# Optimization experiments

Measured on AMD Instinct MI355X. Metric: run time of the kernel, lower is better.

The kernel has to match this reference:

```python
import jax, jax.numpy as jnp
import numpy as np

INPUT_SIZE = 512
LATENT = 256
NUM_PROTOTYPES = 128
NUM_CLASSES = 8
PC = NUM_PROTOTYPES // NUM_CLASSES  # prototypes per class
EPS = 1e-4
LOG_MIN = float(np.log(1e-8))  # clamp bounds for logVar


def setup_inputs() -> dict:
    key = jax.random.key(0)
    ks = jax.random.split(key, 12)
    B = 16384
    s = 0.05
    return {
        "x_tab": jax.random.normal(ks[0], (B, INPUT_SIZE), jnp.float32),
        "t": jax.random.randint(ks[1], (B,), 0, NUM_CLASSES),
        "prototype_vectors": jax.random.normal(ks[2], (NUM_PROTOTYPES, LATENT), jnp.float32),
        "W1": jax.random.normal(ks[3], (2 * LATENT, INPUT_SIZE), jnp.float32) * s,
        "b1": jnp.zeros((2 * LATENT,), jnp.float32),
        "W2": jax.random.normal(ks[4], (2 * LATENT, 2 * LATENT), jnp.float32) * s,
        "b2": jnp.zeros((2 * LATENT,), jnp.float32),
        "Wd1": jax.random.normal(ks[5], (LATENT, LATENT), jnp.float32) * s,
        "bd1": jnp.zeros((LATENT,), jnp.float32),
        "Wd2": jax.random.normal(ks[6], (INPUT_SIZE, LATENT), jnp.float32) * s,
        "bd2": jnp.zeros((INPUT_SIZE,), jnp.float32),
        "W_last": jax.random.normal(ks[7], (1, NUM_PROTOTYPES), jnp.float32) * s,
    }


def reference(x_tab, t, prototype_vectors, W1, b1, W2, b2, Wd1, bd1, Wd2, bd2, W_last):
    B = x_tab.shape[0]
    # encoder MLP: Linear -> ReLU -> Linear, output [B, 2*latent]
    h = jnp.maximum(x_tab @ W1.T + b1, 0.0)
    conv = h @ W2.T + b2
    mu = conv[:, :LATENT]
    logVar = jnp.clip(conv[:, LATENT:], LOG_MIN, -LOG_MIN)
    z = mu  # test=True path: z = mu (deterministic)

    # per-sample indices of the prototypes of the correct class: [B, PC]
    idx = t[:, None] * PC + jnp.arange(PC)[None, :]
    protos = prototype_vectors[idx]  # [B, PC, L] gather

    # cdist (p=2) + log-similarity
    diff = z[:, None, :] - protos  # [B, PC, L]
    d = jnp.sqrt(jnp.sum(diff * diff, axis=-1))  # [B, PC]
    sim = jnp.log((d + 1.0) / (d + EPS))

    # scatter into full [B, P] sparse sim tensor
    full_sim = jnp.zeros((B, NUM_PROTOTYPES), x_tab.dtype).at[
        jnp.arange(B)[:, None], idx].set(sim)

    # KL(N(mu, exp(logVar/2)) || N(p, 1)) per-dim, mean over latent
    var = jnp.exp(logVar)
    kl = jnp.mean(-0.5 * logVar[:, None, :]
                  + 0.5 * (var[:, None, :] + diff * diff)
                  - 0.5, axis=-1)  # [B, PC]
    klw = kl * sim
    mask = (klw > 0).astype(sim.dtype)
    kl_loss = jnp.mean(jnp.sum(klw, axis=1) / jnp.sum(sim * mask, axis=1))

    out = full_sim @ W_last.T  # [B, 1]

    # decoder: Linear -> ReLU -> Linear -> tanh
    dh = jnp.maximum(z @ Wd1.T + bd1, 0.0)
    decoded = jnp.tanh(dh @ Wd2.T + bd2)

    # ortho loss over per-class prototype blocks
    pk = prototype_vectors.reshape(NUM_CLASSES, PC, LATENT)
    pk = pk - jnp.mean(pk, axis=1, keepdims=True)
    gram = jnp.einsum('cil,cjl->cij', pk, pk) - jnp.eye(PC, dtype=pk.dtype)
    ortho_loss = jnp.mean(jnp.sqrt(jnp.sum(gram * gram, axis=(1, 2))))

    return out, decoded, kl_loss, ortho_loss
```

## Files before the change

kernel.cpp:

```cpp
#include <hip/hip_runtime.h>
#include <math.h>

typedef unsigned short u16;
typedef unsigned int   u32;
typedef _Float16 f16;
typedef f16   f16x4 __attribute__((ext_vector_type(4)));
typedef f16   f16x8 __attribute__((ext_vector_type(8)));
typedef float f32x4 __attribute__((ext_vector_type(4)));

#define B_ROWS 16384
#define PC 16
#define EPS_SIM 1e-4f
#define LOG_MIN_F (-18.420680743952367f)
#define KL_IDX  (B_ROWS + B_ROWS * 512)
#define OR_IDX  (KL_IDX + 1)

#define GLD16(gp, lp) __builtin_amdgcn_global_load_lds( \
    (const __attribute__((address_space(1))) void*)(gp), \
    (__attribute__((address_space(3))) void*)(lp), 16, 0, 0)

__device__ __forceinline__ void conv4(const float* __restrict__ src,
                                      f16* __restrict__ dst, int i)
{
    float4 v = ((const float4*)src)[i];
    f16x4 o = { (f16)v.x, (f16)v.y, (f16)v.z, (f16)v.w };
    ((f16x4*)dst)[i] = o;
}

__global__ __launch_bounds__(256)
void prep_kernel(const float* __restrict__ x,   const float* __restrict__ W1,
                 const float* __restrict__ W2,  const float* __restrict__ Wd1,
                 const float* __restrict__ Wd2, const float* __restrict__ protos,
                 f16* __restrict__ x_h,  f16* __restrict__ W1h,
                 f16* __restrict__ W2h,  f16* __restrict__ Wd1h,
                 f16* __restrict__ Wd2h, f16* __restrict__ ph,
                 float* __restrict__ pnorm, float* __restrict__ opart,
                 float* __restrict__ S, float* __restrict__ Mn,
                 float* __restrict__ out)
{
    __shared__ float pk[PC][257];
    __shared__ float red[256];
    int blk = blockIdx.x, t = threadIdx.x;

    if (blk < 8) {
        int c = blk;
        for (int i = t; i < PC * 256; i += 256)
            pk[i >> 8][i & 255] = protos[c * PC * 256 + i];
        __syncthreads();
        float mean = 0.f;
#pragma unroll
        for (int i = 0; i < PC; ++i) mean += pk[i][t];
        mean *= (1.f / (float)PC);
#pragma unroll
        for (int i = 0; i < PC; ++i) pk[i][t] -= mean;
        __syncthreads();
        int i = t >> 4, j = t & 15;
        float gg = 0.f;
#pragma unroll 8
        for (int l = 0; l < 256; ++l) gg = fmaf(pk[i][l], pk[j][l], gg);
        gg -= (i == j) ? 1.f : 0.f;
        red[t] = gg * gg;
        __syncthreads();
        for (int s = 128; s; s >>= 1) { if (t < s) red[t] += red[t + s]; __syncthreads(); }
        if (t == 0) opart[c] = sqrtf(red[0]);
        return;
    }
    int b2 = blk - 8;
    if (b2 < 8192)         conv4(x,   x_h,  b2 * 256 + t);
    else if (b2 < 8448)    conv4(W1,  W1h,  (b2 - 8192) * 256 + t);
    else if (b2 < 8704)    conv4(W2,  W2h,  (b2 - 8448) * 256 + t);
    else if (b2 < 8768)    conv4(Wd1, Wd1h, (b2 - 8704) * 256 + t);
    else if (b2 < 8896)    conv4(Wd2, Wd2h, (b2 - 8768) * 256 + t);
    else if (b2 < 8928)    conv4(protos, ph, (b2 - 8896) * 256 + t);
    else if (b2 < 8930) {
        int tt = (b2 - 8928) * 256 + t;
        int row = tt >> 2, q = tt & 3;
        const float* pr = protos + (size_t)row * 256 + q * 64;
        float s = 0.f;
#pragma unroll
        for (int j = 0; j < 16; ++j) {
            float4 v = *(const float4*)(pr + j * 4);
            float r0 = (float)(f16)v.x, r1 = (float)(f16)v.y;
            float r2 = (float)(f16)v.z, r3 = (float)(f16)v.w;
            s = fmaf(r0, r0, s); s = fmaf(r1, r1, s);
            s = fmaf(r2, r2, s); s = fmaf(r3, r3, s);
        }
        s += __shfl_xor(s, 1, 64);
        s += __shfl_xor(s, 2, 64);
        if (q == 0) pnorm[row] = s;
    } else {
        int i = (b2 - 8930) * 256 + t;
        S[i] = 0.f; Mn[i] = 0.f;
        if (i == 0) out[KL_IDX] = 0.f;
    }
}

template<int MODE, int KK>
__global__ __launch_bounds__(256, 2)
void gemm_mfma(const f16* __restrict__ A, const f16* __restrict__ B,
               const f16* __restrict__ P, const float* __restrict__ bias,
               f16* __restrict__ C16, float* __restrict__ Cf,
               float* __restrict__ Srow, float* __restrict__ Mnorm,
               f16* __restrict__ Xc, int ldc)
{
    __shared__ __align__(16) f16 LA[128][32];
    __shared__ __align__(16) f16 LB[128][32];

    const int t = threadIdx.x, lane = t & 63, wave = t >> 6;
    const int wm = wave >> 1, wn = wave & 1;
    const int bm = blockIdx.x * 128;
    const int y  = blockIdx.y;
    const bool proto = (MODE == 5) && (y == 2);
    const int bn  = y * 128;
    const int bnB = proto ? 0 : bn;
    const f16* Bp = proto ? P : B;
    const int rA = lane & 15, g = lane >> 4;
    const int srow = lane >> 2, cp = lane & 3;

    f32x4 acc[4][4];
    const f32x4 z4 = {0.f, 0.f, 0.f, 0.f};
#pragma unroll
    for (int i = 0; i < 4; ++i)
#pragma unroll
        for (int j = 0; j < 4; ++j) acc[i][j] = z4;

    auto stage = [&](int kt) {
#pragma unroll
        for (int s = 0; s < 2; ++s) {
            int row = wave * 32 + s * 16 + srow;
            int lc  = (cp - (row >> 1)) & 3;
            GLD16(A  + (size_t)(bm  + row) * KK + kt * 32 + lc * 8,
                  &LA[wave * 32 + s * 16][0]);
            GLD16(Bp + (size_t)(bnB + row) * KK + kt * 32 + lc * 8,
                  &LB[wave * 32 + s * 16][0]);
        }
    };

    constexpr int T = KK / 32;
    stage(0);
    for (int tk = 0; tk < T; ++tk) {
        __syncthreads();

        f16x8 a[4], b[4];
#pragma unroll
        for (int i = 0; i < 4; ++i) {
            int m = wm * 64 + i * 16 + rA;
            int c = ((g + (m >> 1)) & 3) * 8;
            a[i] = *(const f16x8*)&LA[m][c];
            int n = wn * 64 + i * 16 + rA;
            int cn = ((g + (n >> 1)) & 3) * 8;
            b[i] = *(const f16x8*)&LB[n][cn];
        }

        __syncthreads();
        if (tk + 1 < T) stage(tk + 1);

#pragma unroll
        for (int i = 0; i < 4; ++i)
#pragma unroll
            for (int j = 0; j < 4; ++j)
                acc[i][j] = __builtin_amdgcn_mfma_f32_16x16x32_f16(a[i], b[j], acc[i][j], 0, 0, 0);
    }

    if (proto) {
#pragma unroll
        for (int i = 0; i < 4; ++i)
#pragma unroll
            for (int r = 0; r < 4; ++r) {
                size_t row = bm + wm * 64 + i * 16 + g * 4 + r;
#pragma unroll
                for (int j = 0; j < 4; ++j) {
                    int col = wn * 64 + j * 16 + rA;
                    Xc[row * 128 + col] = (f16)acc[i][j][r];
                }
            }
        return;
    }

    float bv[4];
#pragma unroll
    for (int j = 0; j < 4; ++j) bv[j] = bias[bn + wn * 64 + j * 16 + rA];

    if (MODE == 4 && y >= 2) {
#pragma unroll
        for (int i = 0; i < 4; ++i)
#pragma unroll
            for (int r = 0; r < 4; ++r) {
                int row = bm + wm * 64 + i * 16 + g * 4 + r;
                float s = 0.f;
#pragma unroll
                for (int j = 0; j < 4; ++j) {
                    float lv = acc[i][j][r] + bv[j];
                    lv = fminf(fmaxf(lv, LOG_MIN_F), -LOG_MIN_F);
                    s += 0.5f * __expf(lv) - 0.5f * lv - 0.5f;
                }
                s += __shfl_xor(s, 1, 64); s += __shfl_xor(s, 2, 64);
                s += __shfl_xor(s, 4, 64); s += __shfl_xor(s, 8, 64);
                if (rA == 0) atomicAdd(&Srow[row], s * (1.f / 256.f));
            }
        return;
    }

#pragma unroll
    for (int i = 0; i < 4; ++i)
#pragma unroll
        for (int r = 0; r < 4; ++r) {
            size_t row = bm + wm * 64 + i * 16 + g * 4 + r;
            float sq = 0.f;
#pragma unroll
            for (int j = 0; j < 4; ++j) {
                int col = bn + wn * 64 + j * 16 + rA;
                float v = acc[i][j][r] + bv[j];
                if (MODE == 0 || MODE == 5) v = fmaxf(v, 0.f);
                if (MODE == 3) {
                    float e = __expf(2.f * v);
                    Cf[row * ldc + col] = 1.f - 2.f / (e + 1.f);
                } else {
                    f16 hv = (f16)v;
                    C16[row * ldc + col] = hv;
                    if (MODE == 4) {
                        float vr = (float)hv;
                        sq = fmaf(vr, vr, sq);
                    }
                }
            }
            if (MODE == 4) {
                sq += __shfl_xor(sq, 1, 64); sq += __shfl_xor(sq, 2, 64);
                sq += __shfl_xor(sq, 4, 64); sq += __shfl_xor(sq, 8, 64);
                if (rA == 0) atomicAdd(&Mnorm[row], sq);
            }
        }
}

__global__ __launch_bounds__(256)
void proto_finish(const f16* __restrict__ Xc, const float* __restrict__ Mnorm,
                  const float* __restrict__ Sr, const int* __restrict__ tcls,
                  const float* __restrict__ pnorm, const float* __restrict__ Wlast,
                  const float* __restrict__ opart,
                  float* __restrict__ out, float* __restrict__ kl_out)
{
    __shared__ float pnS[128], wlS[128], red[4];
    int t = threadIdx.x;
    if (t < 128) { pnS[t] = pnorm[t]; wlS[t] = Wlast[t]; }
    __syncthreads();

    int b = blockIdx.x * 256 + t;
    int cls = tcls[b];
    float Mn = Mnorm[b], Sb = Sr[b];
    const f16* xr = Xc + (size_t)b * 128 + cls * 16;
    f16x8 c0 = *(const f16x8*)xr;
    f16x8 c1 = *(const f16x8*)(xr + 8);

    float num = 0.f, den = 0.f, ov = 0.f;
#pragma unroll
    for (int p = 0; p < 16; ++p) {
        float c  = (p < 8) ? (float)c0[p] : (float)c1[p - 8];
        int  ip  = cls * 16 + p;
        float dd = fmaxf(Mn + pnS[ip] - 2.f * c, 0.f);
        float d  = sqrtf(dd);
        float sim = __logf((d + 1.f) / (d + EPS_SIM));
        float kl  = Sb + dd * (0.5f / 256.f);
        float klw = kl * sim;
        num += klw;
        den += (klw > 0.f) ? sim : 0.f;
        ov  += sim * wlS[ip];
    }
    out[b] = ov;

    float v = num / den;
#pragma unroll
    for (int off = 32; off; off >>= 1) v += __shfl_xor(v, off, 64);
    int lane = t & 63, w = t >> 6;
    if (lane == 0) red[w] = v;
    __syncthreads();
    if (t == 0)
        atomicAdd(kl_out, (red[0] + red[1] + red[2] + red[3]) * (1.f / (float)B_ROWS));
    if (blockIdx.x == 0 && t == 0) {
        float o = 0.f;
#pragma unroll
        for (int c8 = 0; c8 < 8; ++c8) o += opart[c8];
        out[OR_IDX] = o * (1.f / 8.f);
    }
}

extern "C" void kernel_launch(void* const* d_in, const int* in_sizes, int n_in,
                              void* d_out, int out_size, void* d_ws, size_t ws_size,
                              hipStream_t stream)
{
    const float* x      = (const float*)d_in[0];
    const int*   tcls   = (const int*)  d_in[1];
    const float* protos = (const float*)d_in[2];
    const float* W1     = (const float*)d_in[3];
    const float* b1     = (const float*)d_in[4];
    const float* W2     = (const float*)d_in[5];
    const float* b2     = (const float*)d_in[6];
    const float* Wd1    = (const float*)d_in[7];
    const float* bd1    = (const float*)d_in[8];
    const float* Wd2    = (const float*)d_in[9];
    const float* bd2    = (const float*)d_in[10];
    const float* Wlast  = (const float*)d_in[11];

    float* out     = (float*)d_out;
    float* decoded = out + B_ROWS;

    f16* h_h = (f16*)decoded;

    f16* wsf  = (f16*)d_ws;
    f16* x_h  = wsf;
    f16* mu_h = wsf + 8388608;
    f16* dh_h = wsf + 12582912;

    float* S = (float*)((char*)d_ws + 33554432);
    f16* w = (f16*)(S + 32768);
    f16 *W1h = w, *W2h = w + 262144, *Wd1h = w + 524288, *Wd2h = w + 589824;
    f16 *ph  = w + 720896;
    float* munorm = (float*)(w + 753664);
    float* pnorm  = munorm + 16384;
    float* opart  = pnorm + 128;
    f16* Xc = (f16*)((char*)d_ws + 37748736);

    hipLaunchKernelGGL(prep_kernel, dim3(9002), dim3(256), 0, stream,
                       x, W1, W2, Wd1, Wd2, protos,
                       x_h, W1h, W2h, Wd1h, Wd2h, ph,
                       pnorm, opart, S, munorm, out);

    hipLaunchKernelGGL((gemm_mfma<0, 512>), dim3(128, 4), dim3(256), 0, stream,
                       x_h, W1h, (f16*)nullptr, b1,
                       h_h, (float*)nullptr, (float*)nullptr, (float*)nullptr,
                       (f16*)nullptr, 512);
    hipLaunchKernelGGL((gemm_mfma<4, 512>), dim3(128, 4), dim3(256), 0, stream,
                       h_h, W2h, (f16*)nullptr, b2,
                       mu_h, (float*)nullptr, S, munorm,
                       (f16*)nullptr, 256);
    hipLaunchKernelGGL((gemm_mfma<5, 256>), dim3(128, 3), dim3(256), 0, stream,
                       mu_h, Wd1h, ph, bd1,
                       dh_h, (float*)nullptr, (float*)nullptr, (float*)nullptr,
                       Xc, 256);
    hipLaunchKernelGGL(proto_finish, dim3(64), dim3(256), 0, stream,
                       Xc, munorm, S, tcls, pnorm, Wlast, opart,
                       out, out + KL_IDX);
    hipLaunchKernelGGL((gemm_mfma<3, 256>), dim3(128, 4), dim3(256), 0, stream,
                       dh_h, Wd2h, (f16*)nullptr, bd2,
                       (f16*)nullptr, decoded, (float*)nullptr, (float*)nullptr,
                       (f16*)nullptr, 512);
}
```

Baseline: 77.05 us.

## Fuse fp32 input conversion into first GEMM, double-buffer LDS, merge proto_finish

The first GEMM now reads x in fp32 directly and converts it to fp16 into swizzled LDS. This removes the separate x conversion pass and its 16 MB workspace round trip. GEMM tiles shrink to 128x64 with double-buffered LDS, one barrier per k-step and launch bounds raised to 4 blocks per CU, giving more blocks and better overlap. The proto_finish kernel is folded into the decoder GEMM launch as an extra grid row, saving one launch. The trade-offs are A tiles reloaded twice as often, register-staged conversion loads instead of async LDS loads, and extra branching in the GEMM kernel.

```diff
diff --git a/kernel.cpp b/kernel.cpp
--- a/kernel.cpp
+++ b/kernel.cpp
@@ -1,8 +1,6 @@
 #include <hip/hip_runtime.h>
 #include <math.h>
 
-typedef unsigned short u16;
-typedef unsigned int   u32;
 typedef _Float16 f16;
 typedef f16   f16x4 __attribute__((ext_vector_type(4)));
 typedef f16   f16x8 __attribute__((ext_vector_type(8)));
@@ -28,12 +26,12 @@
 }
 
 __global__ __launch_bounds__(256)
-void prep_kernel(const float* __restrict__ x,   const float* __restrict__ W1,
-                 const float* __restrict__ W2,  const float* __restrict__ Wd1,
-                 const float* __restrict__ Wd2, const float* __restrict__ protos,
-                 f16* __restrict__ x_h,  f16* __restrict__ W1h,
-                 f16* __restrict__ W2h,  f16* __restrict__ Wd1h,
-                 f16* __restrict__ Wd2h, f16* __restrict__ ph,
+void prep_kernel(const float* __restrict__ W1,  const float* __restrict__ W2,
+                 const float* __restrict__ Wd1, const float* __restrict__ Wd2,
+                 const float* __restrict__ protos,
+                 f16* __restrict__ W1h,  f16* __restrict__ W2h,
+                 f16* __restrict__ Wd1h, f16* __restrict__ Wd2h,
+                 f16* __restrict__ ph,
                  float* __restrict__ pnorm, float* __restrict__ opart,
                  float* __restrict__ S, float* __restrict__ Mn,
                  float* __restrict__ out)
@@ -66,14 +64,13 @@
         return;
     }
     int b2 = blk - 8;
-    if (b2 < 8192)         conv4(x,   x_h,  b2 * 256 + t);
-    else if (b2 < 8448)    conv4(W1,  W1h,  (b2 - 8192) * 256 + t);
-    else if (b2 < 8704)    conv4(W2,  W2h,  (b2 - 8448) * 256 + t);
-    else if (b2 < 8768)    conv4(Wd1, Wd1h, (b2 - 8704) * 256 + t);
-    else if (b2 < 8896)    conv4(Wd2, Wd2h, (b2 - 8768) * 256 + t);
-    else if (b2 < 8928)    conv4(protos, ph, (b2 - 8896) * 256 + t);
-    else if (b2 < 8930) {
-        int tt = (b2 - 8928) * 256 + t;
+    if (b2 < 256)          conv4(W1,  W1h,  b2 * 256 + t);
+    else if (b2 < 512)     conv4(W2,  W2h,  (b2 - 256) * 256 + t);
+    else if (b2 < 576)     conv4(Wd1, Wd1h, (b2 - 512) * 256 + t);
+    else if (b2 < 704)     conv4(Wd2, Wd2h, (b2 - 576) * 256 + t);
+    else if (b2 < 736)     conv4(protos, ph, (b2 - 704) * 256 + t);
+    else if (b2 < 738) {
+        int tt = (b2 - 736) * 256 + t;
         int row = tt >> 2, q = tt & 3;
         const float* pr = protos + (size_t)row * 256 + q * 64;
         float s = 0.f;
@@ -89,77 +86,175 @@
         s += __shfl_xor(s, 2, 64);
         if (q == 0) pnorm[row] = s;
     } else {
-        int i = (b2 - 8930) * 256 + t;
+        int i = (b2 - 738) * 256 + t;
         S[i] = 0.f; Mn[i] = 0.f;
         if (i == 0) out[KL_IDX] = 0.f;
     }
 }
 
-template<int MODE, int KK>
-__global__ __launch_bounds__(256, 2)
-void gemm_mfma(const f16* __restrict__ A, const f16* __restrict__ B,
-               const f16* __restrict__ P, const float* __restrict__ bias,
+template<int MODE, int KK, int CONV>
+__global__ __launch_bounds__(256, 4)
+void gemm_mfma(const float* __restrict__ A32, const f16* __restrict__ A,
+               const f16* __restrict__ B, const f16* __restrict__ P,
+               const float* __restrict__ bias,
                f16* __restrict__ C16, float* __restrict__ Cf,
                float* __restrict__ Srow, float* __restrict__ Mnorm,
-               f16* __restrict__ Xc, int ldc)
+               f16* __restrict__ Xc,
+               const int* __restrict__ tcls, const float* __restrict__ pnorm,
+               const float* __restrict__ Wlast, const float* __restrict__ opart,
+               float* __restrict__ out, float* __restrict__ kl_out, int ldc)
 {
-    __shared__ __align__(16) f16 LA[128][32];
-    __shared__ __align__(16) f16 LB[128][32];
-
-    const int t = threadIdx.x, lane = t & 63, wave = t >> 6;
+    const int t = threadIdx.x;
+
+    if (MODE == 3 && blockIdx.y == 8) {
+        if (blockIdx.x >= 64) return;
+        __shared__ float pnS[128], wlS[128], redk[4];
+        if (t < 128) { pnS[t] = pnorm[t]; wlS[t] = Wlast[t]; }
+        __syncthreads();
+        int b = blockIdx.x * 256 + t;
+        int cls = tcls[b];
+        float Mn = Mnorm[b], Sb = Srow[b];
+        const f16* xr = Xc + (size_t)b * 128 + cls * 16;
+        f16x8 c0 = *(const f16x8*)xr;
+        f16x8 c1 = *(const f16x8*)(xr + 8);
+        float num = 0.f, den = 0.f, ov = 0.f;
+#pragma unroll
+        for (int p = 0; p < 16; ++p) {
+            float c  = (p < 8) ? (float)c0[p] : (float)c1[p - 8];
+            int  ip  = cls * 16 + p;
+            float dd = fmaxf(Mn + pnS[ip] - 2.f * c, 0.f);
+            float d  = sqrtf(dd);
+            float sim = __logf((d + 1.f) / (d + EPS_SIM));
+            float kl  = Sb + dd * (0.5f / 256.f);
+            float klw = kl * sim;
+            num += klw;
+            den += (klw > 0.f) ? sim : 0.f;
+            ov  += sim * wlS[ip];
+        }
+        out[b] = ov;
+        float v = num / den;
+#pragma unroll
+        for (int off = 32; off; off >>= 1) v += __shfl_xor(v, off, 64);
+        int lane2 = t & 63, w2 = t >> 6;
+        if (lane2 == 0) redk[w2] = v;
+        __syncthreads();
+        if (t == 0)
+            atomicAdd(kl_out, (redk[0] + redk[1] + redk[2] + redk[3]) * (1.f / (float)B_ROWS));
+        if (blockIdx.x == 0 && t == 0) {
+            float o = 0.f;
+#pragma unroll
+            for (int c8 = 0; c8 < 8; ++c8) o += opart[c8];
+            out[OR_IDX] = o * (1.f / 8.f);
+        }
+        return;
+    }
+
+    __shared__ __align__(16) f16 LA[2][128][32];
+    __shared__ __align__(16) f16 LB[2][64][32];
+
+    const int lane = t & 63, wave = t >> 6;
     const int wm = wave >> 1, wn = wave & 1;
     const int bm = blockIdx.x * 128;
     const int y  = blockIdx.y;
-    const bool proto = (MODE == 5) && (y == 2);
-    const int bn  = y * 128;
-    const int bnB = proto ? 0 : bn;
+    const bool proto = (MODE == 5) && (y >= 4);
+    const int bn  = y * 64;
+    const int bnB = proto ? (y - 4) * 64 : bn;
     const f16* Bp = proto ? P : B;
     const int rA = lane & 15, g = lane >> 4;
     const int srow = lane >> 2, cp = lane & 3;
 
-    f32x4 acc[4][4];
+    f32x4 acc[4][2];
     const f32x4 z4 = {0.f, 0.f, 0.f, 0.f};
 #pragma unroll
     for (int i = 0; i < 4; ++i)
 #pragma unroll
-        for (int j = 0; j < 4; ++j) acc[i][j] = z4;
-
-    auto stage = [&](int kt) {
-#pragma unroll
-        for (int s = 0; s < 2; ++s) {
-            int row = wave * 32 + s * 16 + srow;
-            int lc  = (cp - (row >> 1)) & 3;
-            GLD16(A  + (size_t)(bm  + row) * KK + kt * 32 + lc * 8,
-                  &LA[wave * 32 + s * 16][0]);
-            GLD16(Bp + (size_t)(bnB + row) * KK + kt * 32 + lc * 8,
-                  &LB[wave * 32 + s * 16][0]);
-        }
-    };
+        for (int j = 0; j < 2; ++j) acc[i][j] = z4;
 
     constexpr int T = KK / 32;
-    stage(0);
+
+    {
+        int row = wave * 16 + srow;
+        int lc  = (cp - (row >> 1)) & 3;
+        GLD16(Bp + (size_t)(bnB + row) * KK + lc * 8, &LB[0][wave * 16][0]);
+        if (CONV) {
+#pragma unroll
+            for (int s = 0; s < 4; ++s) {
+                int r8 = wave * 32 + s * 8 + (lane >> 3);
+                int h  = lane & 7;
+                float4 v = *(const float4*)(A32 + (size_t)(bm + r8) * KK + h * 4);
+                f16x4 o = {(f16)v.x, (f16)v.y, (f16)v.z, (f16)v.w};
+                *(f16x4*)((char*)&LA[0][r8][0] +
+                          ((((h >> 1) + (r8 >> 1)) & 3) * 16 + (h & 1) * 8)) = o;
+            }
+        } else {
+#pragma unroll
+            for (int s = 0; s < 2; ++s) {
+                int r16 = wave * 32 + s * 16 + srow;
+                int lc2 = (cp - (r16 >> 1)) & 3;
+                GLD16(A + (size_t)(bm + r16) * KK + lc2 * 8,
+                      &LA[0][wave * 32 + s * 16][0]);
+            }
+        }
+    }
+
     for (int tk = 0; tk < T; ++tk) {
-        __syncthreads();
-
-        f16x8 a[4], b[4];
+        const int buf = tk & 1;
+        __syncthreads();
+
+        f16x8 a[4], b[2];
 #pragma unroll
         for (int i = 0; i < 4; ++i) {
             int m = wm * 64 + i * 16 + rA;
             int c = ((g + (m >> 1)) & 3) * 8;
-            a[i] = *(const f16x8*)&LA[m][c];
-            int n = wn * 64 + i * 16 + rA;
-            int cn = ((g + (n >> 1)) & 3) * 8;
-            b[i] = *(const f16x8*)&LB[n][cn];
-        }
-
-        __syncthreads();
-        if (tk + 1 < T) stage(tk + 1);
+            a[i] = *(const f16x8*)&LA[buf][m][c];
+        }
+#pragma unroll
+        for (int j = 0; j < 2; ++j) {
+            int n = wn * 32 + j * 16 + rA;
+            int c = ((g + (n >> 1)) & 3) * 8;
+            b[j] = *(const f16x8*)&LB[buf][n][c];
+        }
+
+        float4 rr[4];
+        if (tk + 1 < T) {
+            int row = wave * 16 + srow;
+            int lc  = (cp - (row >> 1)) & 3;
+            GLD16(Bp + (size_t)(bnB + row) * KK + (tk + 1) * 32 + lc * 8,
+                  &LB[buf ^ 1][wave * 16][0]);
+            if (CONV) {
+#pragma unroll
+                for (int s = 0; s < 4; ++s) {
+                    int r8 = wave * 32 + s * 8 + (lane >> 3);
+                    rr[s] = *(const float4*)(A32 + (size_t)(bm + r8) * KK +
+                                             (tk + 1) * 32 + (lane & 7) * 4);
+                }
+            } else {
+#pragma unroll
+                for (int s = 0; s < 2; ++s) {
+                    int r16 = wave * 32 + s * 16 + srow;
+                    int lc2 = (cp - (r16 >> 1)) & 3;
+                    GLD16(A + (size_t)(bm + r16) * KK + (tk + 1) * 32 + lc2 * 8,
+                          &LA[buf ^ 1][wave * 32 + s * 16][0]);
+                }
+            }
+        }
 
 #pragma unroll
         for (int i = 0; i < 4; ++i)
 #pragma unroll
-            for (int j = 0; j < 4; ++j)
+            for (int j = 0; j < 2; ++j)
                 acc[i][j] = __builtin_amdgcn_mfma_f32_16x16x32_f16(a[i], b[j], acc[i][j], 0, 0, 0);
+
+        if (CONV && tk + 1 < T) {
+#pragma unroll
+            for (int s = 0; s < 4; ++s) {
+                int r8 = wave * 32 + s * 8 + (lane >> 3);
+                int h  = lane & 7;
+                f16x4 o = {(f16)rr[s].x, (f16)rr[s].y, (f16)rr[s].z, (f16)rr[s].w};
+                *(f16x4*)((char*)&LA[buf ^ 1][r8][0] +
+                          ((((h >> 1) + (r8 >> 1)) & 3) * 16 + (h & 1) * 8)) = o;
+            }
+        }
     }
 
     if (proto) {
@@ -169,19 +264,19 @@
             for (int r = 0; r < 4; ++r) {
                 size_t row = bm + wm * 64 + i * 16 + g * 4 + r;
 #pragma unroll
-                for (int j = 0; j < 4; ++j) {
-                    int col = wn * 64 + j * 16 + rA;
+                for (int j = 0; j < 2; ++j) {
+                    int col = (y - 4) * 64 + wn * 32 + j * 16 + rA;
                     Xc[row * 128 + col] = (f16)acc[i][j][r];
                 }
             }
         return;
     }
 
-    float bv[4];
-#pragma unroll
-    for (int j = 0; j < 4; ++j) bv[j] = bias[bn + wn * 64 + j * 16 + rA];
-
-    if (MODE == 4 && y >= 2) {
+    float bv[2];
+#pragma unroll
+    for (int j = 0; j < 2; ++j) bv[j] = bias[bn + wn * 32 + j * 16 + rA];
+
+    if (MODE == 4 && y >= 4) {
 #pragma unroll
         for (int i = 0; i < 4; ++i)
 #pragma unroll
@@ -189,7 +284,7 @@
                 int row = bm + wm * 64 + i * 16 + g * 4 + r;
                 float s = 0.f;
 #pragma unroll
-                for (int j = 0; j < 4; ++j) {
+                for (int j = 0; j < 2; ++j) {
                     float lv = acc[i][j][r] + bv[j];
                     lv = fminf(fmaxf(lv, LOG_MIN_F), -LOG_MIN_F);
                     s += 0.5f * __expf(lv) - 0.5f * lv - 0.5f;
@@ -208,8 +303,8 @@
             size_t row = bm + wm * 64 + i * 16 + g * 4 + r;
             float sq = 0.f;
 #pragma unroll
-            for (int j = 0; j < 4; ++j) {
-                int col = bn + wn * 64 + j * 16 + rA;
+            for (int j = 0; j < 2; ++j) {
+                int col = bn + wn * 32 + j * 16 + rA;
                 float v = acc[i][j][r] + bv[j];
                 if (MODE == 0 || MODE == 5) v = fmaxf(v, 0.f);
                 if (MODE == 3) {
@@ -224,63 +319,12 @@
                     }
                 }
             }
-            if (MODE == 4) {
+            if (MODE == 4 && y < 4) {
                 sq += __shfl_xor(sq, 1, 64); sq += __shfl_xor(sq, 2, 64);
                 sq += __shfl_xor(sq, 4, 64); sq += __shfl_xor(sq, 8, 64);
                 if (rA == 0) atomicAdd(&Mnorm[row], sq);
             }
         }
-}
-
-__global__ __launch_bounds__(256)
-void proto_finish(const f16* __restrict__ Xc, const float* __restrict__ Mnorm,
-                  const float* __restrict__ Sr, const int* __restrict__ tcls,
-                  const float* __restrict__ pnorm, const float* __restrict__ Wlast,
-                  const float* __restrict__ opart,
-                  float* __restrict__ out, float* __restrict__ kl_out)
-{
-    __shared__ float pnS[128], wlS[128], red[4];
-    int t = threadIdx.x;
-    if (t < 128) { pnS[t] = pnorm[t]; wlS[t] = Wlast[t]; }
-    __syncthreads();
-
-    int b = blockIdx.x * 256 + t;
-    int cls = tcls[b];
-    float Mn = Mnorm[b], Sb = Sr[b];
-    const f16* xr = Xc + (size_t)b * 128 + cls * 16;
-    f16x8 c0 = *(const f16x8*)xr;
-    f16x8 c1 = *(const f16x8*)(xr + 8);
-
-    float num = 0.f, den = 0.f, ov = 0.f;
-#pragma unroll
-    for (int p = 0; p < 16; ++p) {
-        float c  = (p < 8) ? (float)c0[p] : (float)c1[p - 8];
-        int  ip  = cls * 16 + p;
-        float dd = fmaxf(Mn + pnS[ip] - 2.f * c, 0.f);
-        float d  = sqrtf(dd);
-        float sim = __logf((d + 1.f) / (d + EPS_SIM));
-        float kl  = Sb + dd * (0.5f / 256.f);
-        float klw = kl * sim;
-        num += klw;
-        den += (klw > 0.f) ? sim : 0.f;
-        ov  += sim * wlS[ip];
-    }
-    out[b] = ov;
-
-    float v = num / den;
-#pragma unroll
-    for (int off = 32; off; off >>= 1) v += __shfl_xor(v, off, 64);
-    int lane = t & 63, w = t >> 6;
-    if (lane == 0) red[w] = v;
-    __syncthreads();
-    if (t == 0)
-        atomicAdd(kl_out, (red[0] + red[1] + red[2] + red[3]) * (1.f / (float)B_ROWS));
-    if (blockIdx.x == 0 && t == 0) {
-        float o = 0.f;
-#pragma unroll
-        for (int c8 = 0; c8 < 8; ++c8) o += opart[c8];
-        out[OR_IDX] = o * (1.f / 8.f);
-    }
 }
 
 extern "C" void kernel_launch(void* const* d_in, const int* in_sizes, int n_in,
@@ -306,41 +350,44 @@
     f16* h_h = (f16*)decoded;
 
     f16* wsf  = (f16*)d_ws;
-    f16* x_h  = wsf;
-    f16* mu_h = wsf + 8388608;
-    f16* dh_h = wsf + 12582912;
-
-    float* S = (float*)((char*)d_ws + 33554432);
-    f16* w = (f16*)(S + 32768);
+    f16* mu_h = wsf;
+    f16* dh_h = wsf + 4194304;
+
+    float* S      = (float*)((char*)d_ws + 16777216);
+    float* munorm = S + 16384;
+    float* pnorm  = munorm + 16384;
+    float* opart  = pnorm + 128;
+    f16* w = (f16*)(opart + 8);
     f16 *W1h = w, *W2h = w + 262144, *Wd1h = w + 524288, *Wd2h = w + 589824;
     f16 *ph  = w + 720896;
-    float* munorm = (float*)(w + 753664);
-    float* pnorm  = munorm + 16384;
-    float* opart  = pnorm + 128;
-    f16* Xc = (f16*)((char*)d_ws + 37748736);
-
-    hipLaunchKernelGGL(prep_kernel, dim3(9002), dim3(256), 0, stream,
-                       x, W1, W2, Wd1, Wd2, protos,
-                       x_h, W1h, W2h, Wd1h, Wd2h, ph,
+    f16* Xc = (f16*)((char*)d_ws + 20971520);
+
+    hipLaunchKernelGGL(prep_kernel, dim3(810), dim3(256), 0, stream,
+                       W1, W2, Wd1, Wd2, protos,
+                       W1h, W2h, Wd1h, Wd2h, ph,
                        pnorm, opart, S, munorm, out);
 
-    hipLaunchKernelGGL((gemm_mfma<0, 512>), dim3(128, 4), dim3(256), 0, stream,
-                       x_h, W1h, (f16*)nullptr, b1,
+    hipLaunchKernelGGL((gemm_mfma<0, 512, 1>), dim3(128, 8), dim3(256), 0, stream,
+                       x, (f16*)nullptr, W1h, (f16*)nullptr, b1,
                        h_h, (float*)nullptr, (float*)nullptr, (float*)nullptr,
-                       (f16*)nullptr, 512);
-    hipLaunchKernelGGL((gemm_mfma<4, 512>), dim3(128, 4), dim3(256), 0, stream,
-                       h_h, W2h, (f16*)nullptr, b2,
+                       (f16*)nullptr, (int*)nullptr, (float*)nullptr,
+                       (float*)nullptr, (float*)nullptr,
+                       (float*)nullptr, (float*)nullptr, 512);
+    hipLaunchKernelGGL((gemm_mfma<4, 512, 0>), dim3(128, 8), dim3(256), 0, stream,
+                       (float*)nullptr, h_h, W2h, (f16*)nullptr, b2,
                        mu_h, (float*)nullptr, S, munorm,
-                       (f16*)nullptr, 256);
-    hipLaunchKernelGGL((gemm_mfma<5, 256>), dim3(128, 3), dim3(256), 0, stream,
-                       mu_h, Wd1h, ph, bd1,
+                       (f16*)nullptr, (int*)nullptr, (float*)nullptr,
+                       (float*)nullptr, (float*)nullptr,
+                       (float*)nullptr, (float*)nullptr, 256);
+    hipLaunchKernelGGL((gemm_mfma<5, 256, 0>), dim3(128, 6), dim3(256), 0, stream,
+                       (float*)nullptr, mu_h, Wd1h, ph, bd1,
                        dh_h, (float*)nullptr, (float*)nullptr, (float*)nullptr,
-                       Xc, 256);
-    hipLaunchKernelGGL(proto_finish, dim3(64), dim3(256), 0, stream,
-                       Xc, munorm, S, tcls, pnorm, Wlast, opart,
-                       out, out + KL_IDX);
-    hipLaunchKernelGGL((gemm_mfma<3, 256>), dim3(128, 4), dim3(256), 0, stream,
-                       dh_h, Wd2h, (f16*)nullptr, bd2,
-                       (f16*)nullptr, decoded, (float*)nullptr, (float*)nullptr,
-                       (f16*)nullptr, 512);
+                       Xc, (int*)nullptr, (float*)nullptr,
+                       (float*)nullptr, (float*)nullptr,
+                       (float*)nullptr, (float*)nullptr, 256);
+    hipLaunchKernelGGL((gemm_mfma<3, 256, 0>), dim3(128, 9), dim3(256), 0, stream,
+                       (float*)nullptr, dh_h, Wd2h, (f16*)nullptr, bd2,
+                       (f16*)nullptr, decoded, S, munorm,
+                       Xc, tcls, pnorm, Wlast, opart,
+                       out, out + KL_IDX, 512);
 }
```

Result: slower. 82.43 us (+7.0%).

## Fuse fp32-to-fp16 conversion of x into first GEMM's A-tile loading

Applied to the files above, without the earlier changes.

The separate prep pass that converted the 16384x512 fp32 input to fp16 in workspace is removed. The first encoder GEMM now loads fp32 rows of x directly into registers, converts them, and writes swizzled fp16 tiles to LDS, prefetching the next tile before the MFMAs. This avoids writing and re-reading a 16 MB fp16 copy, and the workspace layout is compacted to match. The cost is that the first GEMM reads twice the bytes per A tile, and since it is grid-tiled over N (4 column blocks) each x row is read and converted four times, with register-staged loads in place of direct global-to-LDS loads.

```diff
diff --git a/kernel.cpp b/kernel.cpp
--- a/kernel.cpp
+++ b/kernel.cpp
@@ -1,8 +1,6 @@
 #include <hip/hip_runtime.h>
 #include <math.h>
 
-typedef unsigned short u16;
-typedef unsigned int   u32;
 typedef _Float16 f16;
 typedef f16   f16x4 __attribute__((ext_vector_type(4)));
 typedef f16   f16x8 __attribute__((ext_vector_type(8)));
@@ -28,12 +26,12 @@
 }
 
 __global__ __launch_bounds__(256)
-void prep_kernel(const float* __restrict__ x,   const float* __restrict__ W1,
-                 const float* __restrict__ W2,  const float* __restrict__ Wd1,
-                 const float* __restrict__ Wd2, const float* __restrict__ protos,
-                 f16* __restrict__ x_h,  f16* __restrict__ W1h,
-                 f16* __restrict__ W2h,  f16* __restrict__ Wd1h,
-                 f16* __restrict__ Wd2h, f16* __restrict__ ph,
+void prep_kernel(const float* __restrict__ W1,  const float* __restrict__ W2,
+                 const float* __restrict__ Wd1, const float* __restrict__ Wd2,
+                 const float* __restrict__ protos,
+                 f16* __restrict__ W1h,  f16* __restrict__ W2h,
+                 f16* __restrict__ Wd1h, f16* __restrict__ Wd2h,
+                 f16* __restrict__ ph,
                  float* __restrict__ pnorm, float* __restrict__ opart,
                  float* __restrict__ S, float* __restrict__ Mn,
                  float* __restrict__ out)
@@ -66,14 +64,13 @@
         return;
     }
     int b2 = blk - 8;
-    if (b2 < 8192)         conv4(x,   x_h,  b2 * 256 + t);
-    else if (b2 < 8448)    conv4(W1,  W1h,  (b2 - 8192) * 256 + t);
-    else if (b2 < 8704)    conv4(W2,  W2h,  (b2 - 8448) * 256 + t);
-    else if (b2 < 8768)    conv4(Wd1, Wd1h, (b2 - 8704) * 256 + t);
-    else if (b2 < 8896)    conv4(Wd2, Wd2h, (b2 - 8768) * 256 + t);
-    else if (b2 < 8928)    conv4(protos, ph, (b2 - 8896) * 256 + t);
-    else if (b2 < 8930) {
-        int tt = (b2 - 8928) * 256 + t;
+    if (b2 < 256)          conv4(W1,  W1h,  b2 * 256 + t);
+    else if (b2 < 512)     conv4(W2,  W2h,  (b2 - 256) * 256 + t);
+    else if (b2 < 576)     conv4(Wd1, Wd1h, (b2 - 512) * 256 + t);
+    else if (b2 < 704)     conv4(Wd2, Wd2h, (b2 - 576) * 256 + t);
+    else if (b2 < 736)     conv4(protos, ph, (b2 - 704) * 256 + t);
+    else if (b2 < 738) {
+        int tt = (b2 - 736) * 256 + t;
         int row = tt >> 2, q = tt & 3;
         const float* pr = protos + (size_t)row * 256 + q * 64;
         float s = 0.f;
@@ -89,16 +86,17 @@
         s += __shfl_xor(s, 2, 64);
         if (q == 0) pnorm[row] = s;
     } else {
-        int i = (b2 - 8930) * 256 + t;
+        int i = (b2 - 738) * 256 + t;
         S[i] = 0.f; Mn[i] = 0.f;
         if (i == 0) out[KL_IDX] = 0.f;
     }
 }
 
-template<int MODE, int KK>
+template<int MODE, int KK, int CONV>
 __global__ __launch_bounds__(256, 2)
-void gemm_mfma(const f16* __restrict__ A, const f16* __restrict__ B,
-               const f16* __restrict__ P, const float* __restrict__ bias,
+void gemm_mfma(const float* __restrict__ A32, const f16* __restrict__ A,
+               const f16* __restrict__ B, const f16* __restrict__ P,
+               const float* __restrict__ bias,
                f16* __restrict__ C16, float* __restrict__ Cf,
                float* __restrict__ Srow, float* __restrict__ Mnorm,
                f16* __restrict__ Xc, int ldc)
@@ -124,20 +122,50 @@
 #pragma unroll
         for (int j = 0; j < 4; ++j) acc[i][j] = z4;
 
-    auto stage = [&](int kt) {
+    const int cr8 = lane >> 3, ch = lane & 7;
+
+    auto stageB = [&](int kt) {
 #pragma unroll
         for (int s = 0; s < 2; ++s) {
             int row = wave * 32 + s * 16 + srow;
             int lc  = (cp - (row >> 1)) & 3;
-            GLD16(A  + (size_t)(bm  + row) * KK + kt * 32 + lc * 8,
-                  &LA[wave * 32 + s * 16][0]);
             GLD16(Bp + (size_t)(bnB + row) * KK + kt * 32 + lc * 8,
                   &LB[wave * 32 + s * 16][0]);
         }
     };
+    auto stageA = [&](int kt) {
+#pragma unroll
+        for (int s = 0; s < 2; ++s) {
+            int row = wave * 32 + s * 16 + srow;
+            int lc  = (cp - (row >> 1)) & 3;
+            GLD16(A + (size_t)(bm + row) * KK + kt * 32 + lc * 8,
+                  &LA[wave * 32 + s * 16][0]);
+        }
+    };
+    auto writeA = [&](const float4* rr) {
+#pragma unroll
+        for (int s = 0; s < 4; ++s) {
+            int r8 = wave * 32 + s * 8 + cr8;
+            f16x4 o = {(f16)rr[s].x, (f16)rr[s].y, (f16)rr[s].z, (f16)rr[s].w};
+            *(f16x4*)((char*)&LA[r8][0] +
+                      ((((ch >> 1) + (r8 >> 1)) & 3) * 16 + (ch & 1) * 8)) = o;
+        }
+    };
 
     constexpr int T = KK / 32;
-    stage(0);
+    stageB(0);
+    if (CONV) {
+        float4 rr[4];
+#pragma unroll
+        for (int s = 0; s < 4; ++s) {
+            int r8 = wave * 32 + s * 8 + cr8;
+            rr[s] = *(const float4*)(A32 + (size_t)(bm + r8) * KK + ch * 4);
+        }
+        writeA(rr);
+    } else {
+        stageA(0);
+    }
+
     for (int tk = 0; tk < T; ++tk) {
         __syncthreads();
 
@@ -153,13 +181,30 @@
         }
 
         __syncthreads();
-        if (tk + 1 < T) stage(tk + 1);
+
+        float4 rr[4];
+        if (tk + 1 < T) {
+            stageB(tk + 1);
+            if (CONV) {
+#pragma unroll
+                for (int s = 0; s < 4; ++s) {
+                    int r8 = wave * 32 + s * 8 + cr8;
+                    rr[s] = *(const float4*)(A32 + (size_t)(bm + r8) * KK +
+                                             (tk + 1) * 32 + ch * 4);
+                }
+            } else {
+                stageA(tk + 1);
+            }
+        }
 
 #pragma unroll
         for (int i = 0; i < 4; ++i)
 #pragma unroll
             for (int j = 0; j < 4; ++j)
                 acc[i][j] = __builtin_amdgcn_mfma_f32_16x16x32_f16(a[i], b[j], acc[i][j], 0, 0, 0);
+
+        if (CONV && tk + 1 < T)
+            writeA(rr);
     }
 
     if (proto) {
@@ -306,41 +351,40 @@
     f16* h_h = (f16*)decoded;
 
     f16* wsf  = (f16*)d_ws;
-    f16* x_h  = wsf;
-    f16* mu_h = wsf + 8388608;
-    f16* dh_h = wsf + 12582912;
-
-    float* S = (float*)((char*)d_ws + 33554432);
-    f16* w = (f16*)(S + 32768);
+    f16* mu_h = wsf;
+    f16* dh_h = wsf + 4194304;
+
+    float* S      = (float*)((char*)d_ws + 16777216);
+    float* munorm = S + 16384;
+    float* pnorm  = munorm + 16384;
+    float* opart  = pnorm + 128;
+    f16* w = (f16*)(opart + 8);
     f16 *W1h = w, *W2h = w + 262144, *Wd1h = w + 524288, *Wd2h = w + 589824;
     f16 *ph  = w + 720896;
-    float* munorm = (float*)(w + 753664);
-    float* pnorm  = munorm + 16384;
-    float* opart  = pnorm + 128;
-    f16* Xc = (f16*)((char*)d_ws + 37748736);
-
-    hipLaunchKernelGGL(prep_kernel, dim3(9002), dim3(256), 0, stream,
-                       x, W1, W2, Wd1, Wd2, protos,
-                       x_h, W1h, W2h, Wd1h, Wd2h, ph,
+    f16* Xc = (f16*)((char*)d_ws + 20971520);
+
+    hipLaunchKernelGGL(prep_kernel, dim3(810), dim3(256), 0, stream,
+                       W1, W2, Wd1, Wd2, protos,
+                       W1h, W2h, Wd1h, Wd2h, ph,
                        pnorm, opart, S, munorm, out);
 
-    hipLaunchKernelGGL((gemm_mfma<0, 512>), dim3(128, 4), dim3(256), 0, stream,
-                       x_h, W1h, (f16*)nullptr, b1,
+    hipLaunchKernelGGL((gemm_mfma<0, 512, 1>), dim3(128, 4), dim3(256), 0, stream,
+                       x, (f16*)nullptr, W1h, (f16*)nullptr, b1,
                        h_h, (float*)nullptr, (float*)nullptr, (float*)nullptr,
                        (f16*)nullptr, 512);
-    hipLaunchKernelGGL((gemm_mfma<4, 512>), dim3(128, 4), dim3(256), 0, stream,
-                       h_h, W2h, (f16*)nullptr, b2,
+    hipLaunchKernelGGL((gemm_mfma<4, 512, 0>), dim3(128, 4), dim3(256), 0, stream,
+                       (float*)nullptr, h_h, W2h, (f16*)nullptr, b2,
                        mu_h, (float*)nullptr, S, munorm,
                        (f16*)nullptr, 256);
-    hipLaunchKernelGGL((gemm_mfma<5, 256>), dim3(128, 3), dim3(256), 0, stream,
-                       mu_h, Wd1h, ph, bd1,
+    hipLaunchKernelGGL((gemm_mfma<5, 256, 0>), dim3(128, 3), dim3(256), 0, stream,
+                       (float*)nullptr, mu_h, Wd1h, ph, bd1,
                        dh_h, (float*)nullptr, (float*)nullptr, (float*)nullptr,
                        Xc, 256);
     hipLaunchKernelGGL(proto_finish, dim3(64), dim3(256), 0, stream,
                        Xc, munorm, S, tcls, pnorm, Wlast, opart,
                        out, out + KL_IDX);
-    hipLaunchKernelGGL((gemm_mfma<3, 256>), dim3(128, 4), dim3(256), 0, stream,
-                       dh_h, Wd2h, (f16*)nullptr, bd2,
+    hipLaunchKernelGGL((gemm_mfma<3, 256, 0>), dim3(128, 4), dim3(256), 0, stream,
+                       (float*)nullptr, dh_h, Wd2h, (f16*)nullptr, bd2,
                        (f16*)nullptr, decoded, (float*)nullptr, (float*)nullptr,
                        (f16*)nullptr, 512);
 }
```

Result: slower. 83.24 us (+8.0%).
